# Performance work log

Hardware: AMD Instinct MI355X
Metric: run time of the kernel (lower is better)

Reference implementation:

```python
import jax, jax.numpy as jnp
import numpy as np

B, S, EMBED = 8, 2048, 512
FFN = 2048
N_QUBITS = 10
DEPTH = 2


def _apply_1q(state, mats, wire):
    # state: (N,) + (2,)*n complex; mats: (N,2,2) per-token or (2,2) shared
    s = jnp.moveaxis(state, 1 + wire, 1)
    shp = s.shape
    s = s.reshape(shp[0], 2, -1)
    if mats.ndim == 3:
        s = jnp.einsum('nab,nbr->nar', mats, s)
    else:
        s = jnp.einsum('ab,nbr->nar', mats, s)
    return jnp.moveaxis(s.reshape(shp), 1, 1 + wire)


def _cnot(state, ctrl, tgt):
    # CNOT: flip target axis on the control=1 slice
    ca, ta = 1 + ctrl, 1 + tgt
    s0 = jax.lax.index_in_dim(state, 0, axis=ca, keepdims=True)
    s1 = jax.lax.index_in_dim(state, 1, axis=ca, keepdims=True)
    s1 = jnp.flip(s1, axis=ta)
    return jnp.concatenate([s0, s1], axis=ca)


def _qlayer(x_flat, theta, n_qubits=N_QUBITS, depth=DEPTH):
    # x_flat: (N, n_qubits) RX encoding angles; theta: (n_qubits,) RY params
    N = x_flat.shape[0]
    state = jnp.zeros((N,) + (2,) * n_qubits, jnp.complex64)
    state = state.at[(slice(None),) + (0,) * n_qubits].set(1.0)
    # encoder: RX(x_i) on wire i, per-token angles
    for w in range(n_qubits):
        a = x_flat[:, w] * 0.5
        c = jnp.cos(a).astype(jnp.complex64)
        s = (-1j * jnp.sin(a)).astype(jnp.complex64)
        mats = jnp.stack([jnp.stack([c, s], -1), jnp.stack([s, c], -1)], -2)  # (N,2,2)
        state = _apply_1q(state, mats, w)
    # trainable RY(theta_w) on each wire (shared across tokens)
    for w in range(n_qubits):
        a = theta[w] * 0.5
        c, s = jnp.cos(a), jnp.sin(a)
        mat = jnp.stack([jnp.stack([c, -s]), jnp.stack([s, c])]).astype(jnp.complex64)
        state = _apply_1q(state, mat, w)
    # depth rounds of ring CNOT chain
    for _ in range(depth):
        for w in range(n_qubits - 1):
            state = _cnot(state, w, w + 1)
        state = _cnot(state, n_qubits - 1, 0)
    # MeasureAll PauliZ: <Z_w> per wire
    probs = jnp.abs(state.reshape(N, -1)) ** 2  # (N, 2^n)
    bits = (jnp.arange(2 ** n_qubits)[None, :] >> (n_qubits - 1 - jnp.arange(n_qubits))[:, None]) & 1
    z = (1 - 2 * bits).astype(probs.dtype)  # (n, 2^n)
    return probs @ z.T  # (N, n)


def setup_inputs() -> dict:
    key = jax.random.key(0)
    k = jax.random.split(key, 6)
    x = jax.random.normal(k[0], (B, S, EMBED), jnp.float32)
    ry_theta = jax.random.uniform(k[1], (N_QUBITS,), jnp.float32, 0.0, 2.0 * np.pi)
    W1 = jax.random.normal(k[2], (FFN, N_QUBITS), jnp.float32) / np.sqrt(N_QUBITS)
    b1 = jax.random.normal(k[3], (FFN,), jnp.float32) * 0.01
    W2 = jax.random.normal(k[4], (EMBED, FFN), jnp.float32) / np.sqrt(FFN)
    b2 = jax.random.normal(k[5], (EMBED,), jnp.float32) * 0.01
    return {"x": x, "ry_theta": ry_theta, "W1": W1, "b1": b1, "W2": W2, "b2": b2}


def reference(x, ry_theta, W1, b1, W2, b2):
    b, s, _ = x.shape
    xf = x.reshape(b * s, -1)[:, :N_QUBITS]  # encoder only uses first n_qubits feats
    q = _qlayer(xf, ry_theta).reshape(b, s, N_QUBITS)
    # dropout is identity at eval; linear1 -> relu -> linear2
    h = jax.nn.relu(q @ W1.T + b1)
    return h @ W2.T + b2
```

## Files before the change

kernel.cpp:

```cpp
#include <hip/hip_runtime.h>
#include <hip/hip_bf16.h>


typedef __attribute__((ext_vector_type(8))) short bf16x8;
typedef __attribute__((ext_vector_type(16))) float f32x16;
typedef __attribute__((ext_vector_type(8))) unsigned short us8;
typedef unsigned int u32;

#define NTOK  16384
#define EMBED 512
#define FFN   2048
#define NQ    10
#define BM    128
#define BN    64
#define NKT   32

__device__ __forceinline__ unsigned short f2bf(float f) {
  union { float f; unsigned int u; } a; a.f = f;
  unsigned int r = a.u + 0x7FFFu + ((a.u >> 16) & 1u);
  return (unsigned short)(r >> 16);
}

__device__ __forceinline__ void gload_lds16(const void* g, void* l) {
  __builtin_amdgcn_global_load_lds(
      (const __attribute__((address_space(1))) unsigned int*)g,
      (__attribute__((address_space(3))) unsigned int*)l, 16, 0, 0);
}

__global__ __launch_bounds__(256) void k_prep(const float* __restrict__ x,
                                              const float* __restrict__ theta,
                                              const float* __restrict__ W1,
                                              const float* __restrict__ b1,
                                              const float* __restrict__ W2,
                                              unsigned short* __restrict__ W2f,
                                              unsigned short* __restrict__ W1f,
                                              unsigned short* __restrict__ Qf) {
  int bb = blockIdx.x;
  if (bb < 512) {
    int gid = bb * 256 + threadIdx.x;
    int l = gid & 63, kb = (gid >> 6) & 127, tile = gid >> 13;
    int col = tile * 32 + (l & 31);
    int k0 = kb * 16 + (l >> 5) * 8;
    const float* src = W2 + (size_t)col * FFN + k0;
    float4 v0 = *(const float4*)src;
    float4 v1 = *(const float4*)(src + 4);
    us8 o;
    o[0] = f2bf(v0.x); o[1] = f2bf(v0.y); o[2] = f2bf(v0.z); o[3] = f2bf(v0.w);
    o[4] = f2bf(v1.x); o[5] = f2bf(v1.y); o[6] = f2bf(v1.z); o[7] = f2bf(v1.w);
    *(us8*)(W2f + (size_t)gid * 8) = o;
  } else if (bb < 640) {
    int gid = (bb - 512) * 256 + threadIdx.x;
    int l = gid & 63, tile = gid >> 6;
    int tok = tile * 32 + (l & 31), g = l >> 5;
    const int masks[NQ] = {0x2AB,0x3FD,0x3FA,0x3F5,0x3EA,0x3D5,0x3AA,0x355,0x2AA,0x155};
    float z[NQ], qv[NQ];
#pragma unroll
    for (int w = 0; w < NQ; ++w)
      z[w] = __builtin_cosf(x[(size_t)tok * EMBED + w]) * __builtin_cosf(theta[w]);
#pragma unroll
    for (int w = 0; w < NQ; ++w) {
      float p = 1.f;
#pragma unroll
      for (int v = 0; v < NQ; ++v)
        if ((masks[w] >> v) & 1) p *= z[v];
      qv[w] = p;
    }
    us8 o = (us8)0;
    if (g == 0) {
#pragma unroll
      for (int e = 0; e < 8; ++e) o[e] = f2bf(qv[e]);
    } else {
      o[0] = f2bf(qv[8]); o[1] = f2bf(qv[9]); o[2] = f2bf(1.f);
    }
    *(us8*)(Qf + (size_t)gid * 8) = o;
  } else {
    int gid = (bb - 640) * 256 + threadIdx.x;
    int l = gid & 63, blk = gid >> 6;
    int k = blk * 32 + (l & 31);
    int wg = (l >> 5) * 8;
    us8 o;
#pragma unroll
    for (int e = 0; e < 8; ++e) {
      int wire = wg + e;
      float v = (wire < NQ) ? W1[k * NQ + wire] : (wire == NQ ? b1[k] : 0.f);
      o[e] = f2bf(v);
    }
    *(us8*)(W1f + (size_t)gid * 8) = o;
  }
}

__global__ __launch_bounds__(256, 4) void k_fused(const unsigned short* __restrict__ Qf,
                                                  const unsigned short* __restrict__ W1f,
                                                  const unsigned short* __restrict__ W2f,
                                                  const float* __restrict__ b2,
                                                  float* __restrict__ out) {
  __shared__ short Bw[2][8 * 64 * 8];
  __shared__ short W1s[2][2 * 64 * 8];

  int bid = blockIdx.x;
  int swz = (bid & 7) * 128 + (bid >> 3);
  const int m0 = (swz >> 3) * BM;
  const int n0 = (swz & 7) * BN;
  const int tid  = threadIdx.x;
  const int lane = tid & 63;
  const int wave = tid >> 6;
  const int h = lane >> 5, t31 = lane & 31;
  const int nt0 = n0 >> 5;

  bf16x8 qf = *(const bf16x8*)&Qf[(((size_t)(m0 >> 5) + wave) * 64 + lane) * 8];

  f32x16 acc[2] = {};

#define STAGE(KT, B)                                                            \
  { _Pragma("unroll")                                                           \
    for (int hf = 0; hf < 2; ++hf) {                                            \
      int ch = hf * 256 + tid;                                                  \
      int tile2 = ch >> 8, kb = (ch >> 6) & 3, ln = ch & 63;                    \
      gload_lds16(&W2f[(((size_t)(nt0 + tile2) * 128 + (KT) * 4 + kb) * 64 + ln) * 8], \
                  &Bw[B][ch * 8]);                                              \
    }                                                                           \
    if (tid < 128)                                                              \
      gload_lds16(&W1f[(((size_t)(KT) * 2 + (tid >> 6)) * 64 + (tid & 63)) * 8],\
                  &W1s[B][tid * 8]); }

#define HGEN1(WF, AQ0, AQ1)                                                     \
  { f32x16 zz = {};                                                             \
    f32x16 d = __builtin_amdgcn_mfma_f32_32x32x16_bf16((WF), qf, zz, 0, 0, 0);  \
    d = __builtin_elementwise_max(d, zz);                                       \
    u32 dw0, dw1, dw2, dw3, dw4, dw5, dw6, dw7;                                 \
    asm("v_cvt_pk_bf16_f32 %0, %1, %2":"=v"(dw0):"v"(d[0]),"v"(d[1]));          \
    asm("v_cvt_pk_bf16_f32 %0, %1, %2":"=v"(dw1):"v"(d[2]),"v"(d[3]));          \
    asm("v_cvt_pk_bf16_f32 %0, %1, %2":"=v"(dw2):"v"(d[4]),"v"(d[5]));          \
    asm("v_cvt_pk_bf16_f32 %0, %1, %2":"=v"(dw3):"v"(d[6]),"v"(d[7]));          \
    asm("v_cvt_pk_bf16_f32 %0, %1, %2":"=v"(dw4):"v"(d[8]),"v"(d[9]));          \
    asm("v_cvt_pk_bf16_f32 %0, %1, %2":"=v"(dw5):"v"(d[10]),"v"(d[11]));        \
    asm("v_cvt_pk_bf16_f32 %0, %1, %2":"=v"(dw6):"v"(d[12]),"v"(d[13]));        \
    asm("v_cvt_pk_bf16_f32 %0, %1, %2":"=v"(dw7):"v"(d[14]),"v"(d[15]));        \
    asm("v_permlane32_swap_b32 %0, %1" : "+v"(dw0), "+v"(dw2));                 \
    asm("v_permlane32_swap_b32 %0, %1" : "+v"(dw1), "+v"(dw3));                 \
    asm("v_permlane32_swap_b32 %0, %1" : "+v"(dw4), "+v"(dw6));                 \
    asm("v_permlane32_swap_b32 %0, %1" : "+v"(dw5), "+v"(dw7));                 \
    union { u32 u[4]; bf16x8 v; } u0, u1;                                       \
    u0.u[0]=dw0; u0.u[1]=dw1; u0.u[2]=dw2; u0.u[3]=dw3;                         \
    u1.u[0]=dw4; u1.u[1]=dw5; u1.u[2]=dw6; u1.u[3]=dw7;                         \
    AQ0 = u0.v; AQ1 = u1.v; }

  STAGE(0, 0);

  for (int kt = 0; kt < NKT; ++kt) {
    const int cur = kt & 1;
    asm volatile("s_waitcnt vmcnt(0)" ::: "memory");
    __builtin_amdgcn_s_barrier();
    asm volatile("" ::: "memory");
    if (kt + 1 < NKT) STAGE(kt + 1, cur ^ 1);

    bf16x8 wf0 = *(const bf16x8*)&W1s[cur][(0 * 64 + lane) * 8];
    bf16x8 wf1 = *(const bf16x8*)&W1s[cur][(1 * 64 + lane) * 8];
    bf16x8 aq0, aq1, aq2, aq3;
    HGEN1(wf0, aq0, aq1);
    HGEN1(wf1, aq2, aq3);

    bf16x8 bg00 = *(const bf16x8*)&Bw[cur][((0 * 4 + 0) * 64 + lane) * 8];
    bf16x8 bg01 = *(const bf16x8*)&Bw[cur][((0 * 4 + 1) * 64 + lane) * 8];
    bf16x8 bg02 = *(const bf16x8*)&Bw[cur][((0 * 4 + 2) * 64 + lane) * 8];
    bf16x8 bg03 = *(const bf16x8*)&Bw[cur][((0 * 4 + 3) * 64 + lane) * 8];
    bf16x8 bg10 = *(const bf16x8*)&Bw[cur][((1 * 4 + 0) * 64 + lane) * 8];
    bf16x8 bg11 = *(const bf16x8*)&Bw[cur][((1 * 4 + 1) * 64 + lane) * 8];
    bf16x8 bg12 = *(const bf16x8*)&Bw[cur][((1 * 4 + 2) * 64 + lane) * 8];
    bf16x8 bg13 = *(const bf16x8*)&Bw[cur][((1 * 4 + 3) * 64 + lane) * 8];
    acc[0] = __builtin_amdgcn_mfma_f32_32x32x16_bf16(aq0, bg00, acc[0], 0, 0, 0);
    acc[1] = __builtin_amdgcn_mfma_f32_32x32x16_bf16(aq0, bg10, acc[1], 0, 0, 0);
    acc[0] = __builtin_amdgcn_mfma_f32_32x32x16_bf16(aq1, bg01, acc[0], 0, 0, 0);
    acc[1] = __builtin_amdgcn_mfma_f32_32x32x16_bf16(aq1, bg11, acc[1], 0, 0, 0);
    acc[0] = __builtin_amdgcn_mfma_f32_32x32x16_bf16(aq2, bg02, acc[0], 0, 0, 0);
    acc[1] = __builtin_amdgcn_mfma_f32_32x32x16_bf16(aq2, bg12, acc[1], 0, 0, 0);
    acc[0] = __builtin_amdgcn_mfma_f32_32x32x16_bf16(aq3, bg03, acc[0], 0, 0, 0);
    acc[1] = __builtin_amdgcn_mfma_f32_32x32x16_bf16(aq3, bg13, acc[1], 0, 0, 0);
  }

#pragma unroll
  for (int j = 0; j < 2; ++j) {
    const int col = n0 + j * 32 + t31;
    const float bbv = b2[col];
#pragma unroll
    for (int r = 0; r < 16; ++r) {
      int tok = m0 + wave * 32 + (r & 3) + 8 * (r >> 2) + 4 * h;
      out[(size_t)tok * EMBED + col] = acc[j][r] + bbv;
    }
  }
#undef STAGE
#undef HGEN1
}

extern "C" void kernel_launch(void* const* d_in, const int* in_sizes, int n_in,
                              void* d_out, int out_size, void* d_ws, size_t ws_size,
                              hipStream_t stream) {
  const float* x     = (const float*)d_in[0];
  const float* theta = (const float*)d_in[1];
  const float* W1    = (const float*)d_in[2];
  const float* b1    = (const float*)d_in[3];
  const float* W2    = (const float*)d_in[4];
  const float* b2    = (const float*)d_in[5];
  float* out = (float*)d_out;

  char* ws = (char*)d_ws;
  unsigned short* W2f = (unsigned short*)ws;
  unsigned short* W1f = (unsigned short*)(ws + (2u << 20));
  unsigned short* Qfg = (unsigned short*)(ws + (2u << 20) + (64u << 10));

  k_prep <<<656, 256, 0, stream>>>(x, theta, W1, b1, W2, W2f, W1f, Qfg);
  k_fused<<<(NTOK / BM) * (EMBED / BN), 256, 0, stream>>>(Qfg, W1f, W2f, b2, out);
}
```

Before: 55.67 us.

## Software-pipeline hidden-layer generation one k-tile ahead of the W2 GEMM

Restructures the main loop so the first-layer MFMA, ReLU and bf16 packing for k-tile kt+1 are computed while the second-layer GEMM consumes k-tile kt. W1 tiles are staged two steps ahead and the loop is unrolled by two with ping-pong register sets. The goal is to break the serial dependency between hidden generation and the W2 MFMAs so they can interleave. This raises register pressure and adds a prologue.

```diff
diff --git a/kernel.cpp b/kernel.cpp
--- a/kernel.cpp
+++ b/kernel.cpp
@@ -110,72 +110,102 @@
   bf16x8 qf = *(const bf16x8*)&Qf[(((size_t)(m0 >> 5) + wave) * 64 + lane) * 8];
 
   f32x16 acc[2] = {};
-
-#define STAGE(KT, B)                                                            \
+  bf16x8 aqA0, aqA1, aqA2, aqA3;
+  bf16x8 aqB0, aqB1, aqB2, aqB3;
+
+#define STAGE_BW(KT, B)                                                         \
   { _Pragma("unroll")                                                           \
     for (int hf = 0; hf < 2; ++hf) {                                            \
       int ch = hf * 256 + tid;                                                  \
       int tile2 = ch >> 8, kb = (ch >> 6) & 3, ln = ch & 63;                    \
       gload_lds16(&W2f[(((size_t)(nt0 + tile2) * 128 + (KT) * 4 + kb) * 64 + ln) * 8], \
                   &Bw[B][ch * 8]);                                              \
-    }                                                                           \
-    if (tid < 128)                                                              \
+    } }
+
+#define STAGE_W1(KT, S)                                                         \
+  { if (tid < 128)                                                              \
       gload_lds16(&W1f[(((size_t)(KT) * 2 + (tid >> 6)) * 64 + (tid & 63)) * 8],\
-                  &W1s[B][tid * 8]); }
-
-#define HGEN1(WF, AQ0, AQ1)                                                     \
+                  &W1s[S][tid * 8]); }
+
+#define POST(D, AQ0, AQ1)                                                       \
   { f32x16 zz = {};                                                             \
-    f32x16 d = __builtin_amdgcn_mfma_f32_32x32x16_bf16((WF), qf, zz, 0, 0, 0);  \
-    d = __builtin_elementwise_max(d, zz);                                       \
-    u32 dw0, dw1, dw2, dw3, dw4, dw5, dw6, dw7;                                 \
-    asm("v_cvt_pk_bf16_f32 %0, %1, %2":"=v"(dw0):"v"(d[0]),"v"(d[1]));          \
-    asm("v_cvt_pk_bf16_f32 %0, %1, %2":"=v"(dw1):"v"(d[2]),"v"(d[3]));          \
-    asm("v_cvt_pk_bf16_f32 %0, %1, %2":"=v"(dw2):"v"(d[4]),"v"(d[5]));          \
-    asm("v_cvt_pk_bf16_f32 %0, %1, %2":"=v"(dw3):"v"(d[6]),"v"(d[7]));          \
-    asm("v_cvt_pk_bf16_f32 %0, %1, %2":"=v"(dw4):"v"(d[8]),"v"(d[9]));          \
-    asm("v_cvt_pk_bf16_f32 %0, %1, %2":"=v"(dw5):"v"(d[10]),"v"(d[11]));        \
-    asm("v_cvt_pk_bf16_f32 %0, %1, %2":"=v"(dw6):"v"(d[12]),"v"(d[13]));        \
-    asm("v_cvt_pk_bf16_f32 %0, %1, %2":"=v"(dw7):"v"(d[14]),"v"(d[15]));        \
-    asm("v_permlane32_swap_b32 %0, %1" : "+v"(dw0), "+v"(dw2));                 \
-    asm("v_permlane32_swap_b32 %0, %1" : "+v"(dw1), "+v"(dw3));                 \
-    asm("v_permlane32_swap_b32 %0, %1" : "+v"(dw4), "+v"(dw6));                 \
-    asm("v_permlane32_swap_b32 %0, %1" : "+v"(dw5), "+v"(dw7));                 \
+    D = __builtin_elementwise_max(D, zz);                                       \
+    u32 w0, w1, w2, w3, w4, w5, w6, w7;                                         \
+    asm("v_cvt_pk_bf16_f32 %0, %1, %2":"=v"(w0):"v"(D[0]),"v"(D[1]));           \
+    asm("v_cvt_pk_bf16_f32 %0, %1, %2":"=v"(w1):"v"(D[2]),"v"(D[3]));           \
+    asm("v_cvt_pk_bf16_f32 %0, %1, %2":"=v"(w2):"v"(D[4]),"v"(D[5]));           \
+    asm("v_cvt_pk_bf16_f32 %0, %1, %2":"=v"(w3):"v"(D[6]),"v"(D[7]));           \
+    asm("v_cvt_pk_bf16_f32 %0, %1, %2":"=v"(w4):"v"(D[8]),"v"(D[9]));           \
+    asm("v_cvt_pk_bf16_f32 %0, %1, %2":"=v"(w5):"v"(D[10]),"v"(D[11]));         \
+    asm("v_cvt_pk_bf16_f32 %0, %1, %2":"=v"(w6):"v"(D[12]),"v"(D[13]));         \
+    asm("v_cvt_pk_bf16_f32 %0, %1, %2":"=v"(w7):"v"(D[14]),"v"(D[15]));         \
+    asm("v_permlane32_swap_b32 %0, %1" : "+v"(w0), "+v"(w2));                   \
+    asm("v_permlane32_swap_b32 %0, %1" : "+v"(w1), "+v"(w3));                   \
+    asm("v_permlane32_swap_b32 %0, %1" : "+v"(w4), "+v"(w6));                   \
+    asm("v_permlane32_swap_b32 %0, %1" : "+v"(w5), "+v"(w7));                   \
     union { u32 u[4]; bf16x8 v; } u0, u1;                                       \
-    u0.u[0]=dw0; u0.u[1]=dw1; u0.u[2]=dw2; u0.u[3]=dw3;                         \
-    u1.u[0]=dw4; u1.u[1]=dw5; u1.u[2]=dw6; u1.u[3]=dw7;                         \
+    u0.u[0]=w0; u0.u[1]=w1; u0.u[2]=w2; u0.u[3]=w3;                             \
+    u1.u[0]=w4; u1.u[1]=w5; u1.u[2]=w6; u1.u[3]=w7;                             \
     AQ0 = u0.v; AQ1 = u1.v; }
 
-  STAGE(0, 0);
-
-  for (int kt = 0; kt < NKT; ++kt) {
-    const int cur = kt & 1;
-    asm volatile("s_waitcnt vmcnt(0)" ::: "memory");
-    __builtin_amdgcn_s_barrier();
-    asm volatile("" ::: "memory");
-    if (kt + 1 < NKT) STAGE(kt + 1, cur ^ 1);
-
-    bf16x8 wf0 = *(const bf16x8*)&W1s[cur][(0 * 64 + lane) * 8];
-    bf16x8 wf1 = *(const bf16x8*)&W1s[cur][(1 * 64 + lane) * 8];
-    bf16x8 aq0, aq1, aq2, aq3;
-    HGEN1(wf0, aq0, aq1);
-    HGEN1(wf1, aq2, aq3);
-
-    bf16x8 bg00 = *(const bf16x8*)&Bw[cur][((0 * 4 + 0) * 64 + lane) * 8];
-    bf16x8 bg01 = *(const bf16x8*)&Bw[cur][((0 * 4 + 1) * 64 + lane) * 8];
-    bf16x8 bg02 = *(const bf16x8*)&Bw[cur][((0 * 4 + 2) * 64 + lane) * 8];
-    bf16x8 bg03 = *(const bf16x8*)&Bw[cur][((0 * 4 + 3) * 64 + lane) * 8];
-    bf16x8 bg10 = *(const bf16x8*)&Bw[cur][((1 * 4 + 0) * 64 + lane) * 8];
-    bf16x8 bg11 = *(const bf16x8*)&Bw[cur][((1 * 4 + 1) * 64 + lane) * 8];
-    bf16x8 bg12 = *(const bf16x8*)&Bw[cur][((1 * 4 + 2) * 64 + lane) * 8];
-    bf16x8 bg13 = *(const bf16x8*)&Bw[cur][((1 * 4 + 3) * 64 + lane) * 8];
-    acc[0] = __builtin_amdgcn_mfma_f32_32x32x16_bf16(aq0, bg00, acc[0], 0, 0, 0);
-    acc[1] = __builtin_amdgcn_mfma_f32_32x32x16_bf16(aq0, bg10, acc[1], 0, 0, 0);
-    acc[0] = __builtin_amdgcn_mfma_f32_32x32x16_bf16(aq1, bg01, acc[0], 0, 0, 0);
-    acc[1] = __builtin_amdgcn_mfma_f32_32x32x16_bf16(aq1, bg11, acc[1], 0, 0, 0);
-    acc[0] = __builtin_amdgcn_mfma_f32_32x32x16_bf16(aq2, bg02, acc[0], 0, 0, 0);
-    acc[1] = __builtin_amdgcn_mfma_f32_32x32x16_bf16(aq2, bg12, acc[1], 0, 0, 0);
-    acc[0] = __builtin_amdgcn_mfma_f32_32x32x16_bf16(aq3, bg03, acc[0], 0, 0, 0);
-    acc[1] = __builtin_amdgcn_mfma_f32_32x32x16_bf16(aq3, bg13, acc[1], 0, 0, 0);
+#define GEMM(B, U0, U1, U2, U3)                                                 \
+  { bf16x8 bg00 = *(const bf16x8*)&Bw[B][((0 * 4 + 0) * 64 + lane) * 8];        \
+    bf16x8 bg01 = *(const bf16x8*)&Bw[B][((0 * 4 + 1) * 64 + lane) * 8];        \
+    bf16x8 bg02 = *(const bf16x8*)&Bw[B][((0 * 4 + 2) * 64 + lane) * 8];        \
+    bf16x8 bg03 = *(const bf16x8*)&Bw[B][((0 * 4 + 3) * 64 + lane) * 8];        \
+    bf16x8 bg10 = *(const bf16x8*)&Bw[B][((1 * 4 + 0) * 64 + lane) * 8];        \
+    bf16x8 bg11 = *(const bf16x8*)&Bw[B][((1 * 4 + 1) * 64 + lane) * 8];        \
+    bf16x8 bg12 = *(const bf16x8*)&Bw[B][((1 * 4 + 2) * 64 + lane) * 8];        \
+    bf16x8 bg13 = *(const bf16x8*)&Bw[B][((1 * 4 + 3) * 64 + lane) * 8];        \
+    acc[0] = __builtin_amdgcn_mfma_f32_32x32x16_bf16(U0, bg00, acc[0], 0, 0, 0); \
+    acc[1] = __builtin_amdgcn_mfma_f32_32x32x16_bf16(U0, bg10, acc[1], 0, 0, 0); \
+    acc[0] = __builtin_amdgcn_mfma_f32_32x32x16_bf16(U1, bg01, acc[0], 0, 0, 0); \
+    acc[1] = __builtin_amdgcn_mfma_f32_32x32x16_bf16(U1, bg11, acc[1], 0, 0, 0); \
+    acc[0] = __builtin_amdgcn_mfma_f32_32x32x16_bf16(U2, bg02, acc[0], 0, 0, 0); \
+    acc[1] = __builtin_amdgcn_mfma_f32_32x32x16_bf16(U2, bg12, acc[1], 0, 0, 0); \
+    acc[0] = __builtin_amdgcn_mfma_f32_32x32x16_bf16(U3, bg03, acc[0], 0, 0, 0); \
+    acc[1] = __builtin_amdgcn_mfma_f32_32x32x16_bf16(U3, bg13, acc[1], 0, 0, 0); }
+
+#define BODY(KT, BUF, WSL, U0, U1, U2, U3, V0, V1, V2, V3)                      \
+  { asm volatile("s_waitcnt vmcnt(0)" ::: "memory");                            \
+    __builtin_amdgcn_s_barrier();                                               \
+    asm volatile("" ::: "memory");                                              \
+    const bool hasN  = (KT) + 1 < NKT;                                          \
+    const bool hasN2 = (KT) + 2 < NKT;                                          \
+    if (hasN)  STAGE_BW((KT) + 1, (BUF) ^ 1);                                   \
+    if (hasN2) STAGE_W1((KT) + 2, (WSL) ^ 1);                                   \
+    if (hasN) {                                                                 \
+      bf16x8 wf0 = *(const bf16x8*)&W1s[WSL][(0 * 64 + lane) * 8];              \
+      bf16x8 wf1 = *(const bf16x8*)&W1s[WSL][(1 * 64 + lane) * 8];              \
+      f32x16 zz = {};                                                           \
+      f32x16 d0 = __builtin_amdgcn_mfma_f32_32x32x16_bf16(wf0, qf, zz, 0, 0, 0); \
+      f32x16 d1 = __builtin_amdgcn_mfma_f32_32x32x16_bf16(wf1, qf, zz, 0, 0, 0); \
+      POST(d0, V0, V1);                                                         \
+      POST(d1, V2, V3);                                                         \
+      GEMM(BUF, U0, U1, U2, U3);                                                \
+    } else {                                                                    \
+      GEMM(BUF, U0, U1, U2, U3);                                                \
+    } }
+
+  STAGE_W1(0, 0);
+  STAGE_W1(1, 1);
+  STAGE_BW(0, 0);
+  asm volatile("s_waitcnt vmcnt(0)" ::: "memory");
+  __builtin_amdgcn_s_barrier();
+  {
+    bf16x8 wf0 = *(const bf16x8*)&W1s[0][(0 * 64 + lane) * 8];
+    bf16x8 wf1 = *(const bf16x8*)&W1s[0][(1 * 64 + lane) * 8];
+    f32x16 zz = {};
+    f32x16 d0 = __builtin_amdgcn_mfma_f32_32x32x16_bf16(wf0, qf, zz, 0, 0, 0);
+    f32x16 d1 = __builtin_amdgcn_mfma_f32_32x32x16_bf16(wf1, qf, zz, 0, 0, 0);
+    POST(d0, aqA0, aqA1);
+    POST(d1, aqA2, aqA3);
+  }
+
+  for (int p2 = 0; p2 < NKT / 2; ++p2) {
+    const int kt = 2 * p2;
+    BODY(kt,     0, 1, aqA0, aqA1, aqA2, aqA3, aqB0, aqB1, aqB2, aqB3);
+    BODY(kt + 1, 1, 0, aqB0, aqB1, aqB2, aqB3, aqA0, aqA1, aqA2, aqA3);
   }
 
 #pragma unroll
@@ -188,8 +218,11 @@
       out[(size_t)tok * EMBED + col] = acc[j][r] + bbv;
     }
   }
-#undef STAGE
-#undef HGEN1
+#undef STAGE_BW
+#undef STAGE_W1
+#undef POST
+#undef GEMM
+#undef BODY
 }
 
 extern "C" void kernel_launch(void* const* d_in, const int* in_sizes, int n_in,
```

New measurement: 57.78 us. 1.04x slower.
